# Performance work log

Hardware: AMD Instinct MI355X
Metric: run time of the kernel (lower is better)

## Reference

```python
import jax, jax.numpy as jnp
from jax import lax
import numpy as np

B, T, F, H = 2048, 256, 64, 32


def setup_inputs() -> dict:
    key = jax.random.key(0)
    k = jax.random.split(key, 7)
    s_ih = 1.0 / np.sqrt(H)  # PyTorch GRU init scale uniform(-1/sqrt(H), 1/sqrt(H))
    return {
        "x": jax.random.normal(k[0], (B, T, F), dtype=jnp.float32),
        "W_ih": jax.random.uniform(k[1], (3 * H, F), minval=-s_ih, maxval=s_ih, dtype=jnp.float32),
        "W_hh": jax.random.uniform(k[2], (3 * H, H), minval=-s_ih, maxval=s_ih, dtype=jnp.float32),
        "b_ih": jax.random.uniform(k[3], (3 * H,), minval=-s_ih, maxval=s_ih, dtype=jnp.float32),
        "b_hh": jax.random.uniform(k[4], (3 * H,), minval=-s_ih, maxval=s_ih, dtype=jnp.float32),
        "W_head": jax.random.uniform(k[5], (1, H), minval=-s_ih, maxval=s_ih, dtype=jnp.float32),
        "b_head": jax.random.uniform(k[6], (1,), minval=-s_ih, maxval=s_ih, dtype=jnp.float32),
    }


def _gru_last_hidden(x, W_ih, W_hh, b_ih, b_hh):
    # Precompute input-to-gate projections for all timesteps: [B,T,3H] -> [T,B,3H]
    xg = jnp.einsum("btf,gf->btg", x, W_ih) + b_ih
    xg = jnp.moveaxis(xg, 1, 0)

    def step(h, xt):
        hg = h @ W_hh.T + b_hh  # [B,3H]
        xr, xz, xn = jnp.split(xt, 3, axis=-1)  # PyTorch gate order: r, z, n
        hr, hz, hn = jnp.split(hg, 3, axis=-1)
        r = jax.nn.sigmoid(xr + hr)
        z = jax.nn.sigmoid(xz + hz)
        n = jnp.tanh(xn + r * hn)
        h_new = (1.0 - z) * n + z * h
        return h_new, None

    h0 = jnp.zeros((x.shape[0], W_hh.shape[1]), dtype=x.dtype)
    hT, _ = lax.scan(step, h0, xg)
    return hT  # [B,H] == out[:, -1, :]


def reference(x, W_ih, W_hh, b_ih, b_hh, W_head, b_head):
    hT = _gru_last_hidden(x, W_ih, W_hh, b_ih, b_hh)
    y = hT @ W_head.T + b_head  # [B,1]
    return jax.nn.sigmoid(y)
```

## Files before the change

### kernel.cpp

```cpp
#include <hip/hip_runtime.h>
#include <cstdint>


#define TSEQ 256
#define CSTRIDE 104

typedef __attribute__((ext_vector_type(8))) short bf16x8;
typedef __attribute__((ext_vector_type(4))) float f32x4;
union BF8 { unsigned u[4]; bf16x8 v; };

__device__ __forceinline__ unsigned bfr(float f) {
    unsigned u = __float_as_uint(f);
    return u + 0x7fffu + ((u >> 16) & 1u);
}
__device__ __forceinline__ unsigned packhi(unsigned a, unsigned b) {
    return __builtin_amdgcn_perm(b, a, 0x07060302u);
}
__device__ __forceinline__ void cvt2(const float4& f0, const float4& f1,
                                     bf16x8& hi, bf16x8& lo) {
    float f[8] = {f0.x,f0.y,f0.z,f0.w, f1.x,f1.y,f1.z,f1.w};
    BF8 H, L;
    #pragma unroll
    for (int d = 0; d < 4; ++d) {
        float a = f[2*d], b = f[2*d+1];
        unsigned ua = __float_as_uint(a), ub = __float_as_uint(b);
        float ra = a - __uint_as_float(ua & 0xffff0000u);
        float rb = b - __uint_as_float(ub & 0xffff0000u);
        H.u[d] = packhi(ua, ub);
        L.u[d] = packhi(bfr(ra), bfr(rb));
    }
    hi = H.v; lo = L.v;
}
__device__ __forceinline__ float sel4(f32x4 v, int u) {
    float a = (u & 1) ? v[1] : v[0];
    float b = (u & 1) ? v[3] : v[2];
    return (u & 2) ? b : a;
}

#define MFMA16(A, B, C) __builtin_amdgcn_mfma_f32_16x16x32_bf16((A), (B), (C), 0, 0, 0)

#define QBCAST(x, w) ((unsigned)__builtin_amdgcn_update_dpp( \
        0, (int)(x), ((w) | ((w)<<2) | ((w)<<4) | ((w)<<6)), 0xf, 0xf, true))

__device__ __forceinline__ void barrier_nodrain() {
    asm volatile("s_waitcnt lgkmcnt(0)" ::: "memory");
    __builtin_amdgcn_s_barrier();
    asm volatile("" ::: "memory");
}

__global__ __launch_bounds__(256, 1)
void gru_fused(const float* __restrict__ x, const float* __restrict__ W_ih,
               const float* __restrict__ W_hh, const float* __restrict__ b_ih,
               const float* __restrict__ b_hh, const float* __restrict__ W_head,
               const float* __restrict__ b_head, float* __restrict__ out)
{
    __shared__ float xsh[2][2][16 * CSTRIDE];
    const int tid  = threadIdx.x;
    const int wid  = tid >> 6;
    const int lane = tid & 63;
    const int m = lane & 15, q = lane >> 4;
    const int b0 = blockIdx.x * 8;

    if (wid >= 2) {
        const int pq = wid - 2;
        const int bq = m & 3, u = m >> 2;
        bf16x8 Aih[6][2];
        #pragma unroll
        for (int nt = 0; nt < 6; ++nt)
            #pragma unroll
            for (int c = 0; c < 2; ++c) {
                const float* wp = W_ih + (nt*16 + m)*64 + c*32 + q*8;
                BF8 t;
                #pragma unroll
                for (int d = 0; d < 4; ++d) t.u[d] = packhi(bfr(wp[2*d]), bfr(wp[2*d+1]));
                Aih[nt][c] = t.v;
            }
        float4 ring[4];
        const float* xcol = x + ((size_t)(b0 + pq*4 + bq)*TSEQ + u)*64 + q*8;
        auto ldring = [&](int grp) {
            const float* p = xcol + grp*256;
            ring[0] = ((const float4*)p)[0];        ring[1] = ((const float4*)p)[1];
            ring[2] = ((const float4*)(p+32))[0];   ring[3] = ((const float4*)(p+32))[1];
        };
        auto projwrite = [&](int buf) {
            bf16x8 Xh0, Xl0, Xh1, Xl1;
            cvt2(ring[0], ring[1], Xh0, Xl0);
            cvt2(ring[2], ring[3], Xh1, Xl1);
            #pragma unroll
            for (int nt = 0; nt < 6; ++nt) {
                f32x4 a = MFMA16(Aih[nt][0], Xh0, ((f32x4){0.f,0.f,0.f,0.f}));
                a = MFMA16(Aih[nt][0], Xl0, a);
                a = MFMA16(Aih[nt][1], Xh1, a);
                a = MFMA16(Aih[nt][1], Xl1, a);
                *(f32x4*)&xsh[buf][pq][m*CSTRIDE + nt*16 + q*4] = a;
            }
        };
        ldring(0);
        projwrite(0);
        ldring(1);
        barrier_nodrain();
        for (int g = 0; g < 64; ++g) {
            if (g < 63) {
                projwrite((g + 1) & 1);
                ldring(g + 2 < 64 ? g + 2 : 63);
            }
            barrier_nodrain();
        }
    } else {
        const int cq = wid;
        const int bq = m >> 2, u = m & 3;
        bf16x8 Awh[6];
        #pragma unroll
        for (int nt = 0; nt < 6; ++nt) {
            const float* wp = W_hh + (nt*16 + m)*32;
            BF8 t;
            #pragma unroll
            for (int d = 0; d < 4; ++d) {
                int dd = q*4 + d;
                t.u[d] = packhi(bfr(wp[dd]), bfr(wp[dd + 16]));
            }
            Awh[nt] = t.v;
        }
        f32x4 FRZ[4], BN0, BN1;
        #pragma unroll
        for (int nt = 0; nt < 4; ++nt) {
            f32x4 t;
            #pragma unroll
            for (int r = 0; r < 4; ++r) { int g = nt*16 + q*4 + r; t[r] = b_ih[g] + b_hh[g]; }
            FRZ[nt] = t;
        }
        #pragma unroll
        for (int r = 0; r < 4; ++r) { BN0[r] = b_hh[64+q*4+r]; BN1[r] = b_hh[80+q*4+r]; }
        const float fn0 = b_ih[64 + q*4 + u], fn1 = b_ih[80 + q*4 + u];

        unsigned Hd[4] = {0u, 0u, 0u, 0u};
        float hOL = 0.f, hOH = 0.f;
        barrier_nodrain();

        const float KS = -1.4426950408889634f;
        const float KT = -2.8853900817779268f;
        for (int g = 0; g < 64; ++g) {
            const int cbuf = g & 1;
            float xp[4][6];
            #pragma unroll
            for (int s = 0; s < 4; ++s) {
                const float* rp = &xsh[cbuf][cq][(bq + 4*s)*CSTRIDE + q*4 + u];
                #pragma unroll
                for (int nt = 0; nt < 6; ++nt) xp[s][nt] = rp[nt*16];
            }
            #pragma unroll
            for (int s = 0; s < 4; ++s) {
                BF8 bh; bh.u[0]=Hd[0]; bh.u[1]=Hd[1]; bh.u[2]=Hd[2]; bh.u[3]=Hd[3];
                f32x4 a0 = MFMA16(Awh[0], bh.v, FRZ[0]);
                f32x4 a1 = MFMA16(Awh[1], bh.v, FRZ[1]);
                f32x4 a2 = MFMA16(Awh[2], bh.v, FRZ[2]);
                f32x4 a3 = MFMA16(Awh[3], bh.v, FRZ[3]);
                f32x4 a4 = MFMA16(Awh[4], bh.v, BN0);
                f32x4 a5 = MFMA16(Awh[5], bh.v, BN1);

                float er0 = __builtin_amdgcn_exp2f(KS * (xp[s][0] + sel4(a0, u)));
                float er1 = __builtin_amdgcn_exp2f(KS * (xp[s][1] + sel4(a1, u)));
                float ez0 = __builtin_amdgcn_exp2f(KS * (xp[s][2] + sel4(a2, u)));
                float ez1 = __builtin_amdgcn_exp2f(KS * (xp[s][3] + sel4(a3, u)));
                float dr0 = 1.f + er0, dr1 = 1.f + er1;
                float dz0 = 1.f + ez0, dz1 = 1.f + ez1;
                float qr = __builtin_amdgcn_rcpf(dr0 * dr1);
                float qz = __builtin_amdgcn_rcpf(dz0 * dz1);
                float r0 = dr1 * qr, r1 = dr0 * qr;
                float z0 = dz1 * qz, z1 = dz0 * qz;
                float v0 = xp[s][4] + fn0 + r0 * sel4(a4, u);
                float v1 = xp[s][5] + fn1 + r1 * sel4(a5, u);
                float et0 = __builtin_amdgcn_exp2f(KT * fabsf(v0));
                float et1 = __builtin_amdgcn_exp2f(KT * fabsf(v1));
                float dt0 = 1.f + et0, dt1 = 1.f + et1;
                float qt = __builtin_amdgcn_rcpf(dt0 * dt1);
                float t0 = copysignf((1.f - et0) * dt1 * qt, v0);
                float t1 = copysignf((1.f - et1) * dt0 * qt, v1);
                float hNL = t0 + z0 * (hOL - t0);
                float hNH = t1 + z1 * (hOH - t1);
                hOL = hNL; hOH = hNH;

                unsigned pk;
                asm("v_cvt_pk_bf16_f32 %0, %1, %2" : "=v"(pk) : "v"(hNL), "v"(hNH));
                Hd[0] = QBCAST(pk, 0);
                Hd[1] = QBCAST(pk, 1);
                Hd[2] = QBCAST(pk, 2);
                Hd[3] = QBCAST(pk, 3);
            }
            barrier_nodrain();
        }

        float v = hOL * W_head[q*4 + u] + hOH * W_head[16 + q*4 + u];
        float s = 1.f / (1.f + __expf(-(0.f)));
        (void)s;
        v += __shfl_xor(v, 1, 64);
        v += __shfl_xor(v, 2, 64);
        v += __shfl_xor(v, 16, 64);
        v += __shfl_xor(v, 32, 64);
        if (lane < 16 && (lane & 3) == 0) {
            float a = v + b_head[0];
            float e = __builtin_amdgcn_exp2f(-1.4426950408889634f * a);
            out[b0 + cq*4 + (lane >> 2)] = __builtin_amdgcn_rcpf(1.f + e);
        }
    }
}

extern "C" void kernel_launch(void* const* d_in, const int* in_sizes, int n_in,
                              void* d_out, int out_size, void* d_ws, size_t ws_size,
                              hipStream_t stream)
{
    const float* x      = (const float*)d_in[0];
    const float* W_ih   = (const float*)d_in[1];
    const float* W_hh   = (const float*)d_in[2];
    const float* b_ih   = (const float*)d_in[3];
    const float* b_hh   = (const float*)d_in[4];
    const float* W_head = (const float*)d_in[5];
    const float* b_head = (const float*)d_in[6];
    float* out = (float*)d_out;

    gru_fused<<<256, 256, 0, stream>>>(x, W_ih, W_hh, b_ih, b_hh,
                                       W_head, b_head, out);
}
```

Measured before the change: 220.1 us.

## Process eight timesteps per barrier and fold biases into input projection

Producer waves now project two timestep groups per iteration into a doubled shared buffer, so the recurrent waves run 8 steps between barriers instead of 4, halving the number of block barriers. The r/z and n input biases are folded into the projection MFMA accumulator init, which removes the bias adds and the separate n-bias add from the serial recurrence. Gate math is rewritten with packed float2 ops and FMAs to shorten the per-step dependency chain. The cost is more shared memory, more registers for the doubled rings and xp array, and longer producer bursts between barriers.

Result: no change. 222.7 us (+1.2%).

```diff
diff --git a/kernel.cpp b/kernel.cpp
--- a/kernel.cpp
+++ b/kernel.cpp
@@ -4,9 +4,11 @@
 
 #define TSEQ 256
 #define CSTRIDE 104
+#define NGRP 32
 
 typedef __attribute__((ext_vector_type(8))) short bf16x8;
 typedef __attribute__((ext_vector_type(4))) float f32x4;
+typedef __attribute__((ext_vector_type(2))) float f32x2;
 union BF8 { unsigned u[4]; bf16x8 v; };
 
 __device__ __forceinline__ unsigned bfr(float f) {
@@ -54,7 +56,7 @@
                const float* __restrict__ b_hh, const float* __restrict__ W_head,
                const float* __restrict__ b_head, float* __restrict__ out)
 {
-    __shared__ float xsh[2][2][16 * CSTRIDE];
+    __shared__ float xsh[2][2][32 * CSTRIDE];
     const int tid  = threadIdx.x;
     const int wid  = tid >> 6;
     const int lane = tid & 63;
@@ -75,34 +77,58 @@
                 for (int d = 0; d < 4; ++d) t.u[d] = packhi(bfr(wp[2*d]), bfr(wp[2*d+1]));
                 Aih[nt][c] = t.v;
             }
-        float4 ring[4];
+        f32x4 PC[6];
+        #pragma unroll
+        for (int nt = 0; nt < 6; ++nt) {
+            f32x4 t;
+            #pragma unroll
+            for (int r = 0; r < 4; ++r) {
+                int g = nt*16 + q*4 + r;
+                t[r] = (nt < 4) ? (b_ih[g] + b_hh[g]) : b_ih[g];
+            }
+            PC[nt] = t;
+        }
+        float4 ringA[4], ringB[4];
         const float* xcol = x + ((size_t)(b0 + pq*4 + bq)*TSEQ + u)*64 + q*8;
-        auto ldring = [&](int grp) {
-            const float* p = xcol + grp*256;
-            ring[0] = ((const float4*)p)[0];        ring[1] = ((const float4*)p)[1];
-            ring[2] = ((const float4*)(p+32))[0];   ring[3] = ((const float4*)(p+32))[1];
+        auto ldrings = [&](int grp) {
+            const float* p0 = xcol + grp*512;
+            const float* p1 = p0 + 256;
+            ringA[0] = ((const float4*)p0)[0];        ringA[1] = ((const float4*)p0)[1];
+            ringA[2] = ((const float4*)(p0+32))[0];   ringA[3] = ((const float4*)(p0+32))[1];
+            ringB[0] = ((const float4*)p1)[0];        ringB[1] = ((const float4*)p1)[1];
+            ringB[2] = ((const float4*)(p1+32))[0];   ringB[3] = ((const float4*)(p1+32))[1];
         };
-        auto projwrite = [&](int buf) {
+        auto projwrite2 = [&](int buf) {
             bf16x8 Xh0, Xl0, Xh1, Xl1;
-            cvt2(ring[0], ring[1], Xh0, Xl0);
-            cvt2(ring[2], ring[3], Xh1, Xl1);
+            cvt2(ringA[0], ringA[1], Xh0, Xl0);
+            cvt2(ringA[2], ringA[3], Xh1, Xl1);
             #pragma unroll
             for (int nt = 0; nt < 6; ++nt) {
-                f32x4 a = MFMA16(Aih[nt][0], Xh0, ((f32x4){0.f,0.f,0.f,0.f}));
+                f32x4 a = MFMA16(Aih[nt][0], Xh0, PC[nt]);
                 a = MFMA16(Aih[nt][0], Xl0, a);
                 a = MFMA16(Aih[nt][1], Xh1, a);
                 a = MFMA16(Aih[nt][1], Xl1, a);
                 *(f32x4*)&xsh[buf][pq][m*CSTRIDE + nt*16 + q*4] = a;
             }
+            cvt2(ringB[0], ringB[1], Xh0, Xl0);
+            cvt2(ringB[2], ringB[3], Xh1, Xl1);
+            #pragma unroll
+            for (int nt = 0; nt < 6; ++nt) {
+                f32x4 a = MFMA16(Aih[nt][0], Xh0, PC[nt]);
+                a = MFMA16(Aih[nt][0], Xl0, a);
+                a = MFMA16(Aih[nt][1], Xh1, a);
+                a = MFMA16(Aih[nt][1], Xl1, a);
+                *(f32x4*)&xsh[buf][pq][(16 + m)*CSTRIDE + nt*16 + q*4] = a;
+            }
         };
-        ldring(0);
-        projwrite(0);
-        ldring(1);
+        ldrings(0);
+        projwrite2(0);
+        ldrings(1);
         barrier_nodrain();
-        for (int g = 0; g < 64; ++g) {
-            if (g < 63) {
-                projwrite((g + 1) & 1);
-                ldring(g + 2 < 64 ? g + 2 : 63);
+        for (int g = 0; g < NGRP; ++g) {
+            if (g < NGRP - 1) {
+                projwrite2((g + 1) & 1);
+                ldrings(g + 2 < NGRP ? g + 2 : NGRP - 1);
             }
             barrier_nodrain();
         }
@@ -121,40 +147,32 @@
             }
             Awh[nt] = t.v;
         }
-        f32x4 FRZ[4], BN0, BN1;
-        #pragma unroll
-        for (int nt = 0; nt < 4; ++nt) {
-            f32x4 t;
-            #pragma unroll
-            for (int r = 0; r < 4; ++r) { int g = nt*16 + q*4 + r; t[r] = b_ih[g] + b_hh[g]; }
-            FRZ[nt] = t;
-        }
+        const f32x4 CZ = {0.f, 0.f, 0.f, 0.f};
+        f32x4 BN0, BN1;
         #pragma unroll
         for (int r = 0; r < 4; ++r) { BN0[r] = b_hh[64+q*4+r]; BN1[r] = b_hh[80+q*4+r]; }
-        const float fn0 = b_ih[64 + q*4 + u], fn1 = b_ih[80 + q*4 + u];
-
-        unsigned Hd[4] = {0u, 0u, 0u, 0u};
-        float hOL = 0.f, hOH = 0.f;
+
+        BF8 bh; bh.u[0]=0u; bh.u[1]=0u; bh.u[2]=0u; bh.u[3]=0u;
+        f32x2 hO = {0.f, 0.f};
         barrier_nodrain();
 
         const float KS = -1.4426950408889634f;
         const float KT = -2.8853900817779268f;
-        for (int g = 0; g < 64; ++g) {
+        for (int g = 0; g < NGRP; ++g) {
             const int cbuf = g & 1;
-            float xp[4][6];
-            #pragma unroll
-            for (int s = 0; s < 4; ++s) {
+            float xp[8][6];
+            #pragma unroll
+            for (int s = 0; s < 8; ++s) {
                 const float* rp = &xsh[cbuf][cq][(bq + 4*s)*CSTRIDE + q*4 + u];
                 #pragma unroll
                 for (int nt = 0; nt < 6; ++nt) xp[s][nt] = rp[nt*16];
             }
             #pragma unroll
-            for (int s = 0; s < 4; ++s) {
-                BF8 bh; bh.u[0]=Hd[0]; bh.u[1]=Hd[1]; bh.u[2]=Hd[2]; bh.u[3]=Hd[3];
-                f32x4 a0 = MFMA16(Awh[0], bh.v, FRZ[0]);
-                f32x4 a1 = MFMA16(Awh[1], bh.v, FRZ[1]);
-                f32x4 a2 = MFMA16(Awh[2], bh.v, FRZ[2]);
-                f32x4 a3 = MFMA16(Awh[3], bh.v, FRZ[3]);
+            for (int s = 0; s < 8; ++s) {
+                f32x4 a0 = MFMA16(Awh[0], bh.v, CZ);
+                f32x4 a1 = MFMA16(Awh[1], bh.v, CZ);
+                f32x4 a2 = MFMA16(Awh[2], bh.v, CZ);
+                f32x4 a3 = MFMA16(Awh[3], bh.v, CZ);
                 f32x4 a4 = MFMA16(Awh[4], bh.v, BN0);
                 f32x4 a5 = MFMA16(Awh[5], bh.v, BN1);
 
@@ -162,37 +180,34 @@
                 float er1 = __builtin_amdgcn_exp2f(KS * (xp[s][1] + sel4(a1, u)));
                 float ez0 = __builtin_amdgcn_exp2f(KS * (xp[s][2] + sel4(a2, u)));
                 float ez1 = __builtin_amdgcn_exp2f(KS * (xp[s][3] + sel4(a3, u)));
-                float dr0 = 1.f + er0, dr1 = 1.f + er1;
-                float dz0 = 1.f + ez0, dz1 = 1.f + ez1;
-                float qr = __builtin_amdgcn_rcpf(dr0 * dr1);
-                float qz = __builtin_amdgcn_rcpf(dz0 * dz1);
-                float r0 = dr1 * qr, r1 = dr0 * qr;
-                float z0 = dz1 * qz, z1 = dz0 * qz;
-                float v0 = xp[s][4] + fn0 + r0 * sel4(a4, u);
-                float v1 = xp[s][5] + fn1 + r1 * sel4(a5, u);
+                f32x2 dr = (f32x2){er0, er1} + 1.f;
+                f32x2 dz = (f32x2){ez0, ez1} + 1.f;
+                float qr = __builtin_amdgcn_rcpf(dr[0] * dr[1]);
+                float qz = __builtin_amdgcn_rcpf(dz[0] * dz[1]);
+                f32x2 rg = (f32x2){dr[1], dr[0]} * qr;
+                f32x2 zg = (f32x2){dz[1], dz[0]} * qz;
+                float v0 = __builtin_fmaf(rg[0], sel4(a4, u), xp[s][4]);
+                float v1 = __builtin_fmaf(rg[1], sel4(a5, u), xp[s][5]);
                 float et0 = __builtin_amdgcn_exp2f(KT * fabsf(v0));
                 float et1 = __builtin_amdgcn_exp2f(KT * fabsf(v1));
-                float dt0 = 1.f + et0, dt1 = 1.f + et1;
-                float qt = __builtin_amdgcn_rcpf(dt0 * dt1);
-                float t0 = copysignf((1.f - et0) * dt1 * qt, v0);
-                float t1 = copysignf((1.f - et1) * dt0 * qt, v1);
-                float hNL = t0 + z0 * (hOL - t0);
-                float hNH = t1 + z1 * (hOH - t1);
-                hOL = hNL; hOH = hNH;
+                f32x2 dt = (f32x2){et0, et1} + 1.f;
+                float qt = __builtin_amdgcn_rcpf(dt[0] * dt[1]);
+                float t0 = copysignf((1.f - et0) * dt[1] * qt, v0);
+                float t1 = copysignf((1.f - et1) * dt[0] * qt, v1);
+                f32x2 tt = {t0, t1};
+                hO = tt + zg * (hO - tt);
 
                 unsigned pk;
-                asm("v_cvt_pk_bf16_f32 %0, %1, %2" : "=v"(pk) : "v"(hNL), "v"(hNH));
-                Hd[0] = QBCAST(pk, 0);
-                Hd[1] = QBCAST(pk, 1);
-                Hd[2] = QBCAST(pk, 2);
-                Hd[3] = QBCAST(pk, 3);
+                asm("v_cvt_pk_bf16_f32 %0, %1, %2" : "=v"(pk) : "v"(hO[0]), "v"(hO[1]));
+                bh.u[0] = QBCAST(pk, 0);
+                bh.u[1] = QBCAST(pk, 1);
+                bh.u[2] = QBCAST(pk, 2);
+                bh.u[3] = QBCAST(pk, 3);
             }
             barrier_nodrain();
         }
 
-        float v = hOL * W_head[q*4 + u] + hOH * W_head[16 + q*4 + u];
-        float s = 1.f / (1.f + __expf(-(0.f)));
-        (void)s;
+        float v = hO[0] * W_head[q*4 + u] + hO[1] * W_head[16 + q*4 + u];
         v += __shfl_xor(v, 1, 64);
         v += __shfl_xor(v, 2, 64);
         v += __shfl_xor(v, 16, 64);
```
